# Performance work log

Measured on AMD Instinct MI355X. Metric: run time of the kernel, lower is better.

## Reference

```python
import jax, jax.numpy as jnp
import numpy as np

B, T, C = 2, 2048, 1024
H, D = 16, 64          # n_heads, head_dim
E, K, HD = 8, 2, 1536  # num_experts, active_experts, expert hidden (int(1.5*C))
EPS = 1e-6


def setup_inputs() -> dict:
    key = jax.random.key(0)
    ks = jax.random.split(key, 13)
    s = 0.02
    return {
        "x": jax.random.normal(ks[0], (B, T, C), jnp.float32),
        "rope_cos": jax.random.uniform(ks[1], (T, D), jnp.float32),
        "rope_sin": jax.random.uniform(ks[2], (T, D), jnp.float32),
        "attn_norm_w": jnp.ones((C,), jnp.float32),
        "q_w": jax.random.normal(ks[3], (C, C), jnp.float32) * s,
        "k_w": jax.random.normal(ks[4], (C, C), jnp.float32) * s,
        "v_w": jax.random.normal(ks[5], (C, C), jnp.float32) * s,
        "o_w": jax.random.normal(ks[6], (C, C), jnp.float32) * s,
        "ffn_norm_w": jnp.ones((C,), jnp.float32),
        "router_w": jax.random.normal(ks[7], (E, C), jnp.float32) * s,
        "w1": jax.random.normal(ks[8], (E, HD, C), jnp.float32) * s,
        "w2": jax.random.normal(ks[9], (E, C, HD), jnp.float32) * s,
        "w3": jax.random.normal(ks[10], (E, HD, C), jnp.float32) * s,
    }


def rmsnorm(x, w):
    var = jnp.mean(x * x, axis=-1, keepdims=True)
    return w * x * jax.lax.rsqrt(var + EPS)


def apply_rope(x, cos, sin):
    # x: [B, T, H, D]; cos/sin: [T, D]
    cos = cos[None, :, None, :]
    sin = sin[None, :, None, :]
    d = x.shape[-1] // 2
    x1, x2 = x[..., :d], x[..., d:]
    rotated = jnp.concatenate([-x2, x1], axis=-1)
    return x * cos + rotated * sin


def reference(x, rope_cos, rope_sin, attn_norm_w, q_w, k_w, v_w, o_w,
              ffn_norm_w, router_w, w1, w2, w3):
    b, t, c = x.shape
    h = rmsnorm(x, attn_norm_w)
    q = (h @ q_w.T).reshape(b, t, H, D)
    k = (h @ k_w.T).reshape(b, t, H, D)
    v = (h @ v_w.T).reshape(b, t, H, D)
    q = apply_rope(q, rope_cos[:t], rope_sin[:t]).transpose(0, 2, 1, 3)  # [B,H,T,D]
    k = apply_rope(k, rope_cos[:t], rope_sin[:t]).transpose(0, 2, 1, 3)
    v = v.transpose(0, 2, 1, 3)
    scores = jnp.einsum('bhqd,bhkd->bhqk', q, k) / jnp.sqrt(jnp.asarray(D, q.dtype))
    causal = jnp.tril(jnp.ones((t, t), bool))
    scores = jnp.where(causal, scores, -jnp.inf)
    attn = jax.nn.softmax(scores, axis=-1)
    y = jnp.einsum('bhqk,bhkd->bhqd', attn, v)
    y = y.transpose(0, 2, 1, 3).reshape(b, t, c)
    x = x + y @ o_w.T

    # Sparse MoE (top-K routing, per-expert SwiGLU, weighted combine)
    hn = rmsnorm(x, ffn_norm_w)
    flat = hn.reshape(-1, c)                                # [N, C]
    logits = flat @ router_w.T                              # [N, E]
    wk, idx = jax.lax.top_k(logits, K)                      # [N, K]
    wk = jax.nn.softmax(wk, axis=-1)
    # combined per-expert gate: [N, E] (zero for unrouted experts)
    gate = jnp.sum((idx[..., None] == jnp.arange(E)) * wk[..., None], axis=1)
    out = jnp.zeros_like(flat)
    for e in range(E):
        g = jax.nn.silu(flat @ w1[e].T) * (flat @ w3[e].T)  # [N, HD]
        out = out + gate[:, e:e + 1] * (g @ w2[e].T)
    return x + out.reshape(b, t, c)
```

## Files before the change

### kernel.cpp

```cpp
#include <hip/hip_runtime.h>
#include <hip/hip_bf16.h>
#include <math.h>

#define Bq 2
#define Tq 2048
#define Cq 1024
#define Hq 16
#define Dq 64
#define Eq 8
#define HDq 1536
#define NTOK (Bq*Tq)

typedef unsigned short u16;
typedef _Float16 f16;
typedef __bf16 bf16x8 __attribute__((ext_vector_type(8)));
typedef _Float16 f16x8 __attribute__((ext_vector_type(8)));
typedef float f32x4v __attribute__((ext_vector_type(4)));

#define MB(x) ((size_t)(x) * 262144)

__device__ __forceinline__ float silu_f(float a) {
    return a / (1.0f + __expf(-a));
}
__device__ __forceinline__ u16 f2bf(float f) {
    union { float f; unsigned u; } a; a.f = f;
    unsigned r = a.u + 0x7fffu + ((a.u >> 16) & 1u);
    return (u16)(r >> 16);
}
__device__ __forceinline__ u16 f16bits(f16 h) {
    union { f16 f; u16 u; } a; a.f = h; return a.u;
}

__device__ __forceinline__ void stage16(const void* g, void* l) {
    __builtin_amdgcn_global_load_lds(
        (const __attribute__((address_space(1))) unsigned int*)g,
        (__attribute__((address_space(3))) unsigned int*)l, 16, 0, 0);
}

__global__ __launch_bounds__(256) void rmsnorm_split_k(const float* __restrict__ x,
                                                       const float* __restrict__ w,
                                                       u16* __restrict__ hh,
                                                       u16* __restrict__ hl) {
    int row = blockIdx.x;
    int tid = threadIdx.x;
    const float* xr = x + (size_t)row * Cq;
    float4 v = *(const float4*)(xr + tid * 4);
    float ss = v.x*v.x + v.y*v.y + v.z*v.z + v.w*v.w;
    #pragma unroll
    for (int off = 32; off; off >>= 1) ss += __shfl_xor(ss, off);
    __shared__ float red[4];
    if ((tid & 63) == 0) red[tid >> 6] = ss;
    __syncthreads();
    float tot = red[0] + red[1] + red[2] + red[3];
    float scale = rsqrtf(tot * (1.0f / (float)Cq) + 1e-6f);
    float4 wv = *(const float4*)(w + tid * 4);
    float o[4] = { v.x*wv.x*scale, v.y*wv.y*scale, v.z*wv.z*scale, v.w*wv.w*scale };
    ushort4 oh, ol;
    u16* ph = (u16*)&oh; u16* pl = (u16*)&ol;
    #pragma unroll
    for (int i = 0; i < 4; i++) {
        f16 hi = (f16)o[i]; f16 lo = (f16)(o[i] - (float)hi);
        ph[i] = f16bits(hi); pl[i] = f16bits(lo);
    }
    *(ushort4*)(hh + (size_t)row * Cq + tid * 4) = oh;
    *(ushort4*)(hl + (size_t)row * Cq + tid * 4) = ol;
}

__global__ __launch_bounds__(256) void rmsnorm2_k(const float* __restrict__ x,
                                                  const float* __restrict__ w,
                                                  float* __restrict__ hn,
                                                  u16* __restrict__ hnb) {
    int row = blockIdx.x;
    int tid = threadIdx.x;
    const float* xr = x + (size_t)row * Cq;
    float4 v = *(const float4*)(xr + tid * 4);
    float ss = v.x*v.x + v.y*v.y + v.z*v.z + v.w*v.w;
    #pragma unroll
    for (int off = 32; off; off >>= 1) ss += __shfl_xor(ss, off);
    __shared__ float red[4];
    if ((tid & 63) == 0) red[tid >> 6] = ss;
    __syncthreads();
    float tot = red[0] + red[1] + red[2] + red[3];
    float scale = rsqrtf(tot * (1.0f / (float)Cq) + 1e-6f);
    float4 wv = *(const float4*)(w + tid * 4);
    float4 o = make_float4(v.x*wv.x*scale, v.y*wv.y*scale, v.z*wv.z*scale, v.w*wv.w*scale);
    *(float4*)(hn + (size_t)row * Cq + tid * 4) = o;
    ushort4 ob = make_ushort4(f2bf(o.x), f2bf(o.y), f2bf(o.z), f2bf(o.w));
    *(ushort4*)(hnb + (size_t)row * Cq + tid * 4) = ob;
}

__global__ __launch_bounds__(256, 3) void gemm_fused(const u16* __restrict__ Ahg,
                                                     const u16* __restrict__ Alg,
                                                     const float* __restrict__ Wq,
                                                     const float* __restrict__ Wk,
                                                     const float* __restrict__ Wv,
                                                     u16* __restrict__ qh_o,
                                                     u16* __restrict__ ql_o,
                                                     u16* __restrict__ kh_o,
                                                     u16* __restrict__ kl_o,
                                                     float* __restrict__ vf_o,
                                                     const float* __restrict__ cosb,
                                                     const float* __restrict__ sinb,
                                                     const float* __restrict__ aux,
                                                     float* __restrict__ outf,
                                                     int kind) {
    __shared__ u16 AhS[2][128*32], AlS[2][128*32], BhS[128*32], BlS[128*32];
    int tid = threadIdx.x;
    int wave = tid >> 6, lane = tid & 63;
    int wm = wave >> 1, wn = wave & 1;
    int bx = blockIdx.x, by = blockIdx.y;
    int proj, nx;
    const float* W;
    if (kind == 0) {
        proj = bx >> 3; nx = bx & 7;
        W = (proj == 0) ? Wq : ((proj == 1) ? Wk : Wv);
    } else {
        proj = 3; nx = bx; W = Wq;
    }

    int srow = tid >> 2, sch = (tid & 3) * 8;
    const u16* A0 = Ahg + (size_t)(by*128 + srow) * Cq + sch;
    const u16* A1 = A0 + (size_t)64 * Cq;
    const u16* L0 = Alg + (size_t)(by*128 + srow) * Cq + sch;
    const u16* L1 = L0 + (size_t)64 * Cq;
    const float* W0 = W + (size_t)(nx*128 + srow) * Cq + sch;
    const float* W1 = W0 + (size_t)64 * Cq;
    int lo0 = srow*32 + sch, lo1 = lo0 + 2048;

    f32x4v acc[4][4];
    #pragma unroll
    for (int i = 0; i < 4; i++)
        #pragma unroll
        for (int j = 0; j < 4; j++)
            #pragma unroll
            for (int r = 0; r < 4; r++) acc[i][j][r] = 0.0f;

    float wr0[8], wr1[8];
    stage16(A0, &AhS[0][lo0]);
    stage16(A1, &AhS[0][lo1]);
    stage16(L0, &AlS[0][lo0]);
    stage16(L1, &AlS[0][lo1]);
    *(float4*)&wr0[0] = *(const float4*)(W0);
    *(float4*)&wr0[4] = *(const float4*)(W0 + 4);
    *(float4*)&wr1[0] = *(const float4*)(W1);
    *(float4*)&wr1[4] = *(const float4*)(W1 + 4);

    int fr = lane & 15, fk = (lane >> 4) * 8;
    int cur = 0;
    for (int k0 = 0; k0 < Cq; k0 += 32, cur ^= 1) {
        __syncthreads();
        {
            f16x8 bh0, bl0, bh1, bl1;
            #pragma unroll
            for (int i = 0; i < 8; i++) {
                f16 h0 = (f16)wr0[i]; bh0[i] = h0; bl0[i] = (f16)(wr0[i] - (float)h0);
                f16 h1 = (f16)wr1[i]; bh1[i] = h1; bl1[i] = (f16)(wr1[i] - (float)h1);
            }
            *(f16x8*)(void*)&BhS[lo0] = bh0;
            *(f16x8*)(void*)&BlS[lo0] = bl0;
            *(f16x8*)(void*)&BhS[lo1] = bh1;
            *(f16x8*)(void*)&BlS[lo1] = bl1;
        }
        __syncthreads();
        int kn = k0 + 32;
        if (kn < Cq) {
            stage16(A0 + kn, &AhS[cur^1][lo0]);
            stage16(A1 + kn, &AhS[cur^1][lo1]);
            stage16(L0 + kn, &AlS[cur^1][lo0]);
            stage16(L1 + kn, &AlS[cur^1][lo1]);
            *(float4*)&wr0[0] = *(const float4*)(W0 + kn);
            *(float4*)&wr0[4] = *(const float4*)(W0 + kn + 4);
            *(float4*)&wr1[0] = *(const float4*)(W1 + kn);
            *(float4*)&wr1[4] = *(const float4*)(W1 + kn + 4);
        }
        f16x8 ah[4], al[4];
        #pragma unroll
        for (int mi = 0; mi < 4; mi++) {
            ah[mi] = *(const f16x8*)(const void*)&AhS[cur][(wm*64 + mi*16 + fr)*32 + fk];
            al[mi] = *(const f16x8*)(const void*)&AlS[cur][(wm*64 + mi*16 + fr)*32 + fk];
        }
        #pragma unroll
        for (int ni = 0; ni < 4; ni++) {
            f16x8 bhf = *(const f16x8*)(const void*)&BhS[(wn*64 + ni*16 + fr)*32 + fk];
            f16x8 blf = *(const f16x8*)(const void*)&BlS[(wn*64 + ni*16 + fr)*32 + fk];
            #pragma unroll
            for (int mi = 0; mi < 4; mi++) {
                acc[mi][ni] = __builtin_amdgcn_mfma_f32_16x16x32_f16(ah[mi], bhf, acc[mi][ni], 0, 0, 0);
                acc[mi][ni] = __builtin_amdgcn_mfma_f32_16x16x32_f16(ah[mi], blf, acc[mi][ni], 0, 0, 0);
                acc[mi][ni] = __builtin_amdgcn_mfma_f32_16x16x32_f16(al[mi], bhf, acc[mi][ni], 0, 0, 0);
            }
        }
    }

    int cr = (lane >> 4) * 4, cc = lane & 15;
    if (proj < 2) {
        u16* dh = (proj == 0) ? qh_o : kh_o;
        u16* dl = (proj == 0) ? ql_o : kl_o;
        float scale = (proj == 0) ? 0.125f : 1.0f;
        int hd = (nx * 2 + wn) * 64;
        #pragma unroll
        for (int mi = 0; mi < 4; mi++)
            #pragma unroll
            for (int r = 0; r < 4; r++) {
                int row = by*128 + wm*64 + mi*16 + cr + r;
                int t = row & (Tq - 1);
                #pragma unroll
                for (int ni = 0; ni < 2; ni++) {
                    int d0 = ni*16 + cc;
                    float a = acc[mi][ni][r];
                    float b = acc[mi][ni+2][r];
                    float c0 = cosb[t*Dq + d0],      s0 = sinb[t*Dq + d0];
                    float c1 = cosb[t*Dq + d0 + 32], s1 = sinb[t*Dq + d0 + 32];
                    float oa = (a * c0 - b * s0) * scale;
                    float ob = (b * c1 + a * s1) * scale;
                    size_t off = (size_t)row * Cq + hd + d0;
                    f16 ha = (f16)oa;
                    f16 hb = (f16)ob;
                    dh[off]      = f16bits(ha);
                    dl[off]      = f16bits((f16)(oa - (float)ha));
                    dh[off + 32] = f16bits(hb);
                    dl[off + 32] = f16bits((f16)(ob - (float)hb));
                }
            }
    } else if (proj == 2) {
        #pragma unroll
        for (int mi = 0; mi < 4; mi++)
            #pragma unroll
            for (int r = 0; r < 4; r++) {
                int row = by*128 + wm*64 + mi*16 + cr + r;
                #pragma unroll
                for (int ni = 0; ni < 4; ni++)
                    vf_o[(size_t)row * Cq + nx*128 + wn*64 + ni*16 + cc] = acc[mi][ni][r];
            }
    } else {
        #pragma unroll
        for (int mi = 0; mi < 4; mi++)
            #pragma unroll
            for (int r = 0; r < 4; r++) {
                int row = by*128 + wm*64 + mi*16 + cr + r;
                #pragma unroll
                for (int ni = 0; ni < 4; ni++) {
                    size_t off = (size_t)row * Cq + nx*128 + wn*64 + ni*16 + cc;
                    outf[off] = acc[mi][ni][r] + aux[off];
                }
            }
    }
}

__global__ __launch_bounds__(256) void vtrans_k(const float* __restrict__ v,
                                                u16* __restrict__ vth,
                                                u16* __restrict__ vtl) {
    __shared__ u16 Th[64 * 72];
    __shared__ u16 Tl[64 * 72];
    int tc = blockIdx.x;
    int bh = blockIdx.y;
    int b = bh >> 4, h = bh & 15;
    int tid = threadIdx.x;
    int tr = tid >> 2;
    int dc = (tid & 3) * 16;
    size_t gin = ((size_t)(b * Tq + tc * 64 + tr)) * Cq + h * Dq + dc;
    #pragma unroll
    for (int i = 0; i < 16; i += 4) {
        float4 f = *(const float4*)(v + gin + i);
        float fv[4] = {f.x, f.y, f.z, f.w};
        #pragma unroll
        for (int j = 0; j < 4; j++) {
            f16 hi = (f16)fv[j];
            f16 lo = (f16)(fv[j] - (float)hi);
            Th[(dc + i + j) * 72 + tr] = f16bits(hi);
            Tl[(dc + i + j) * 72 + tr] = f16bits(lo);
        }
    }
    __syncthreads();
    int dr = tid >> 2;
    int cc = (tid & 3) * 16;
    size_t gout = ((size_t)(bh * 64 + dr)) * Tq + tc * 64 + cc;
    *(uint4*)(vth + gout)     = *(uint4*)(Th + dr * 72 + cc);
    *(uint4*)(vth + gout + 8) = *(uint4*)(Th + dr * 72 + cc + 8);
    *(uint4*)(vtl + gout)     = *(uint4*)(Tl + dr * 72 + cc);
    *(uint4*)(vtl + gout + 8) = *(uint4*)(Tl + dr * 72 + cc + 8);
}

#define AST 72
__global__ __launch_bounds__(256, 2) void attn_f16(const u16* __restrict__ qh_g,
                                                   const u16* __restrict__ ql_g,
                                                   const u16* __restrict__ kh_g,
                                                   const u16* __restrict__ kl_g,
                                                   const u16* __restrict__ vth_g,
                                                   const u16* __restrict__ vtl_g,
                                                   u16* __restrict__ yh_g,
                                                   u16* __restrict__ yl_g) {
    __shared__ u16 Qh[64*AST], Ql[64*AST];
    __shared__ u16 Kh[64*AST], Kl[64*AST];
    __shared__ u16 Vh[64*AST], Vl[64*AST];
    __shared__ u16 Ph[64*AST], Pl[64*AST];

    int j  = blockIdx.x;
    int bh = blockIdx.y;
    int b = bh >> 4, h = bh & 15;
    int tid = threadIdx.x;
    int wv = tid >> 6, lane = tid & 63;
    int fr = lane & 15, fg = lane >> 4;
    int sr = tid >> 2, sc = (tid & 3) * 16;
    int aoff = (wv * 16 + fr) * AST + fg * 8;

    uint4 rkh0, rkh1, rkl0, rkl1, rvh0, rvh1, rvl0, rvl1;
    auto ldkv = [&](int kt) {
        size_t kg = ((size_t)(b * Tq + kt * 64 + sr)) * Cq + h * Dq + sc;
        size_t vg = ((size_t)(bh * 64 + sr)) * Tq + kt * 64 + sc;
        rkh0 = *(const uint4*)(kh_g + kg);  rkh1 = *(const uint4*)(kh_g + kg + 8);
        rkl0 = *(const uint4*)(kl_g + kg);  rkl1 = *(const uint4*)(kl_g + kg + 8);
        rvh0 = *(const uint4*)(vth_g + vg); rvh1 = *(const uint4*)(vth_g + vg + 8);
        rvl0 = *(const uint4*)(vtl_g + vg); rvl1 = *(const uint4*)(vtl_g + vg + 8);
    };

    #pragma unroll
    for (int pass = 0; pass < 2; pass++) {
        int qt = pass == 0 ? (31 - j) : j;

        __syncthreads();
        {
            size_t g = ((size_t)(b * Tq + qt * 64 + sr)) * Cq + h * Dq + sc;
            *(uint4*)(Qh + sr*AST + sc)     = *(const uint4*)(qh_g + g);
            *(uint4*)(Qh + sr*AST + sc + 8) = *(const uint4*)(qh_g + g + 8);
            *(uint4*)(Ql + sr*AST + sc)     = *(const uint4*)(ql_g + g);
            *(uint4*)(Ql + sr*AST + sc + 8) = *(const uint4*)(ql_g + g + 8);
        }
        ldkv(0);

        f32x4v acc_o[4];
        float m_i[4], l_i[4];
        #pragma unroll
        for (int i = 0; i < 4; i++) {
            m_i[i] = -1e30f; l_i[i] = 0.0f;
            #pragma unroll
            for (int r = 0; r < 4; r++) acc_o[i][r] = 0.0f;
        }

        for (int kt = 0; kt <= qt; kt++) {
            __syncthreads();
            *(uint4*)(Kh + sr*AST + sc)     = rkh0;
            *(uint4*)(Kh + sr*AST + sc + 8) = rkh1;
            *(uint4*)(Kl + sr*AST + sc)     = rkl0;
            *(uint4*)(Kl + sr*AST + sc + 8) = rkl1;
            *(uint4*)(Vh + sr*AST + sc)     = rvh0;
            *(uint4*)(Vh + sr*AST + sc + 8) = rvh1;
            *(uint4*)(Vl + sr*AST + sc)     = rvl0;
            *(uint4*)(Vl + sr*AST + sc + 8) = rvl1;
            __syncthreads();
            if (kt < qt) ldkv(kt + 1);

            f16x8 aqh0 = *(const f16x8*)(const void*)(Qh + aoff);
            f16x8 aqh1 = *(const f16x8*)(const void*)(Qh + aoff + 32);
            f16x8 aql0 = *(const f16x8*)(const void*)(Ql + aoff);
            f16x8 aql1 = *(const f16x8*)(const void*)(Ql + aoff + 32);

            f32x4v s[4];
            #pragma unroll
            for (int ni = 0; ni < 4; ni++) {
                int boff = (ni * 16 + fr) * AST + fg * 8;
                f16x8 kh0 = *(const f16x8*)(const void*)(Kh + boff);
                f16x8 kh1 = *(const f16x8*)(const void*)(Kh + boff + 32);
                f16x8 kl0 = *(const f16x8*)(const void*)(Kl + boff);
                f16x8 kl1 = *(const f16x8*)(const void*)(Kl + boff + 32);
                f32x4v t;
                #pragma unroll
                for (int r = 0; r < 4; r++) t[r] = 0.0f;
                t = __builtin_amdgcn_mfma_f32_16x16x32_f16(aqh0, kh0, t, 0, 0, 0);
                t = __builtin_amdgcn_mfma_f32_16x16x32_f16(aqh1, kh1, t, 0, 0, 0);
                t = __builtin_amdgcn_mfma_f32_16x16x32_f16(aqh0, kl0, t, 0, 0, 0);
                t = __builtin_amdgcn_mfma_f32_16x16x32_f16(aqh1, kl1, t, 0, 0, 0);
                t = __builtin_amdgcn_mfma_f32_16x16x32_f16(aql0, kh0, t, 0, 0, 0);
                t = __builtin_amdgcn_mfma_f32_16x16x32_f16(aql1, kh1, t, 0, 0, 0);
                s[ni] = t;
            }

            if (kt == qt) {
                #pragma unroll
                for (int ni = 0; ni < 4; ni++) {
                    int col = ni * 16 + fr;
                    #pragma unroll
                    for (int r = 0; r < 4; r++) {
                        int row = wv * 16 + fg * 4 + r;
                        if (col > row) s[ni][r] = -1e30f;
                    }
                }
            }

            float p[4][4];
            #pragma unroll
            for (int r = 0; r < 4; r++) {
                float mx = fmaxf(fmaxf(s[0][r], s[1][r]), fmaxf(s[2][r], s[3][r]));
                #pragma unroll
                for (int off = 1; off < 16; off <<= 1)
                    mx = fmaxf(mx, __shfl_xor(mx, off, 16));
                float mn = fmaxf(m_i[r], mx);
                float rs = 0.0f;
                #pragma unroll
                for (int ni = 0; ni < 4; ni++) {
                    p[ni][r] = __expf(s[ni][r] - mn);
                    rs += p[ni][r];
                }
                #pragma unroll
                for (int off = 1; off < 16; off <<= 1)
                    rs += __shfl_xor(rs, off, 16);
                float alpha = __expf(m_i[r] - mn);
                l_i[r] = l_i[r] * alpha + rs;
                m_i[r] = mn;
                #pragma unroll
                for (int ni = 0; ni < 4; ni++) acc_o[ni][r] *= alpha;
            }

            #pragma unroll
            for (int ni = 0; ni < 4; ni++) {
                #pragma unroll
                for (int r = 0; r < 4; r++) {
                    int off = (wv * 16 + fg * 4 + r) * AST + ni * 16 + fr;
                    f16 ph = (f16)p[ni][r];
                    f16 pl = (f16)(p[ni][r] - (float)ph);
                    Ph[off] = f16bits(ph);
                    Pl[off] = f16bits(pl);
                }
            }

            f16x8 aph0 = *(const f16x8*)(const void*)(Ph + aoff);
            f16x8 aph1 = *(const f16x8*)(const void*)(Ph + aoff + 32);
            f16x8 apl0 = *(const f16x8*)(const void*)(Pl + aoff);
            f16x8 apl1 = *(const f16x8*)(const void*)(Pl + aoff + 32);
            #pragma unroll
            for (int ni = 0; ni < 4; ni++) {
                int boff = (ni * 16 + fr) * AST + fg * 8;
                f16x8 vh0 = *(const f16x8*)(const void*)(Vh + boff);
                f16x8 vh1 = *(const f16x8*)(const void*)(Vh + boff + 32);
                f16x8 vl0 = *(const f16x8*)(const void*)(Vl + boff);
                f16x8 vl1 = *(const f16x8*)(const void*)(Vl + boff + 32);
                f32x4v t = acc_o[ni];
                t = __builtin_amdgcn_mfma_f32_16x16x32_f16(aph0, vh0, t, 0, 0, 0);
                t = __builtin_amdgcn_mfma_f32_16x16x32_f16(aph1, vh1, t, 0, 0, 0);
                t = __builtin_amdgcn_mfma_f32_16x16x32_f16(aph0, vl0, t, 0, 0, 0);
                t = __builtin_amdgcn_mfma_f32_16x16x32_f16(aph1, vl1, t, 0, 0, 0);
                t = __builtin_amdgcn_mfma_f32_16x16x32_f16(apl0, vh0, t, 0, 0, 0);
                t = __builtin_amdgcn_mfma_f32_16x16x32_f16(apl1, vh1, t, 0, 0, 0);
                acc_o[ni] = t;
            }
        }

        #pragma unroll
        for (int r = 0; r < 4; r++) {
            float inv = 1.0f / l_i[r];
            int row = qt * 64 + wv * 16 + fg * 4 + r;
            size_t base = ((size_t)(b * Tq + row)) * Cq + h * Dq + fr;
            #pragma unroll
            for (int ni = 0; ni < 4; ni++) {
                float yv = acc_o[ni][r] * inv;
                f16 hi = (f16)yv;
                f16 lo = (f16)(yv - (float)hi);
                yh_g[base + ni * 16] = f16bits(hi);
                yl_g[base + ni * 16] = f16bits(lo);
            }
        }
    }
}

__global__ void zero_k(int* cnt) {
    if (threadIdx.x < Eq) cnt[threadIdx.x] = 0;
}

__global__ __launch_bounds__(64) void router_k(const float* __restrict__ hn,
                                               const float* __restrict__ rw,
                                               int* __restrict__ cnt,
                                               int* __restrict__ idxl,
                                               float* __restrict__ gvl) {
    int tkn = blockIdx.x;
    int lane = threadIdx.x;
    float acc[Eq] = {};
    for (int it = 0; it < Cq / 64; it++) {
        float hv = hn[(size_t)tkn * Cq + it * 64 + lane];
        #pragma unroll
        for (int e = 0; e < Eq; e++)
            acc[e] = fmaf(hv, rw[e * Cq + it * 64 + lane], acc[e]);
    }
    #pragma unroll
    for (int e = 0; e < Eq; e++) {
        #pragma unroll
        for (int off = 32; off; off >>= 1) acc[e] += __shfl_xor(acc[e], off);
    }
    int i0 = 0;
    #pragma unroll
    for (int e = 1; e < Eq; e++) if (acc[e] > acc[i0]) i0 = e;
    int i1 = (i0 == 0) ? 1 : 0;
    #pragma unroll
    for (int e = 0; e < Eq; e++)
        if (e != i0 && acc[e] > acc[i1]) i1 = e;
    float p1 = __expf(acc[i1] - acc[i0]);
    float g0 = 1.0f / (1.0f + p1);
    float g1 = p1 / (1.0f + p1);
    if (lane == 0) {
        int p0 = atomicAdd(&cnt[i0], 1);
        idxl[i0 * NTOK + p0] = tkn;
        gvl[i0 * NTOK + p0] = g0;
        int p1i = atomicAdd(&cnt[i1], 1);
        idxl[i1 * NTOK + p1i] = tkn;
        gvl[i1 * NTOK + p1i] = g1;
    }
}

__global__ void setup_k(const int* __restrict__ cnt, int* __restrict__ seg,
                        int* __restrict__ texp, int* __restrict__ ttot) {
    if (threadIdx.x == 0) {
        int base = 0;
        for (int e = 0; e < Eq; e++) {
            seg[e] = base * 128;
            int t = (cnt[e] + 127) >> 7;
            for (int i = 0; i < t; i++) texp[base + i] = e;
            base += t;
        }
        *ttot = base;
    }
}

__global__ __launch_bounds__(256, 2) void moe_w13(const u16* __restrict__ hnb,
                                                  const float* __restrict__ w1,
                                                  const float* __restrict__ w3,
                                                  u16* __restrict__ gbuf,
                                                  const int* __restrict__ cnt,
                                                  const int* __restrict__ seg,
                                                  const int* __restrict__ texp,
                                                  const int* __restrict__ ttot,
                                                  const int* __restrict__ idxl) {
    int by = blockIdx.y;
    if (by >= *ttot) return;
    int e = texp[by];
    const float* w1e = w1 + (size_t)e * HDq * Cq;
    const float* w3e = w3 + (size_t)e * HDq * Cq;
    int cnte = cnt[e], sege = seg[e];
    const int* idxe = idxl + e * NTOK;

    __shared__ u16 As[2][128*32], B1S[128*32], B3S[128*32];
    int tid = threadIdx.x;
    int wave = tid >> 6, lane = tid & 63;
    int wm = wave >> 1, wn = wave & 1;
    int bx = blockIdx.x;
    int srow = tid >> 2, sch = (tid & 3) * 8;

    int r0 = by*128 + srow, r1 = r0 + 64;
    int li0 = r0 - sege, li1 = r1 - sege;
    int tok0 = idxe[li0 < cnte ? li0 : 0];
    int tok1 = idxe[li1 < cnte ? li1 : 0];
    const u16* A0 = hnb + (size_t)tok0 * Cq + sch;
    const u16* A1 = hnb + (size_t)tok1 * Cq + sch;
    const float* W10 = w1e + (size_t)(bx*128 + srow) * Cq + sch;
    const float* W11 = W10 + (size_t)64 * Cq;
    const float* W30 = w3e + (size_t)(bx*128 + srow) * Cq + sch;
    const float* W31 = W30 + (size_t)64 * Cq;
    int lo0 = srow*32 + sch, lo1 = lo0 + 2048;

    f32x4v acc1[4][4], acc3[4][4];
    #pragma unroll
    for (int i = 0; i < 4; i++)
        #pragma unroll
        for (int j = 0; j < 4; j++)
            #pragma unroll
            for (int r = 0; r < 4; r++) { acc1[i][j][r] = 0.0f; acc3[i][j][r] = 0.0f; }

    float x1a[8], x1b[8], x3a[8], x3b[8];
    stage16(A0, &As[0][lo0]);
    stage16(A1, &As[0][lo1]);
    *(float4*)&x1a[0] = *(const float4*)(W10);
    *(float4*)&x1a[4] = *(const float4*)(W10 + 4);
    *(float4*)&x1b[0] = *(const float4*)(W11);
    *(float4*)&x1b[4] = *(const float4*)(W11 + 4);
    *(float4*)&x3a[0] = *(const float4*)(W30);
    *(float4*)&x3a[4] = *(const float4*)(W30 + 4);
    *(float4*)&x3b[0] = *(const float4*)(W31);
    *(float4*)&x3b[4] = *(const float4*)(W31 + 4);

    int fr = lane & 15, fk = (lane >> 4) * 8;
    int cur = 0;
    for (int k0 = 0; k0 < Cq; k0 += 32, cur ^= 1) {
        __syncthreads();
        {
            u16 t0[8], t1[8], t2[8], t3[8];
            #pragma unroll
            for (int i = 0; i < 8; i++) {
                t0[i] = f2bf(x1a[i]); t1[i] = f2bf(x1b[i]);
                t2[i] = f2bf(x3a[i]); t3[i] = f2bf(x3b[i]);
            }
            *(uint4*)&B1S[lo0] = *(uint4*)t0;
            *(uint4*)&B1S[lo1] = *(uint4*)t1;
            *(uint4*)&B3S[lo0] = *(uint4*)t2;
            *(uint4*)&B3S[lo1] = *(uint4*)t3;
        }
        __syncthreads();
        int kn = k0 + 32;
        if (kn < Cq) {
            stage16(A0 + kn, &As[cur^1][lo0]);
            stage16(A1 + kn, &As[cur^1][lo1]);
            *(float4*)&x1a[0] = *(const float4*)(W10 + kn);
            *(float4*)&x1a[4] = *(const float4*)(W10 + kn + 4);
            *(float4*)&x1b[0] = *(const float4*)(W11 + kn);
            *(float4*)&x1b[4] = *(const float4*)(W11 + kn + 4);
            *(float4*)&x3a[0] = *(const float4*)(W30 + kn);
            *(float4*)&x3a[4] = *(const float4*)(W30 + kn + 4);
            *(float4*)&x3b[0] = *(const float4*)(W31 + kn);
            *(float4*)&x3b[4] = *(const float4*)(W31 + kn + 4);
        }
        bf16x8 af[4];
        #pragma unroll
        for (int mi = 0; mi < 4; mi++)
            af[mi] = *(const bf16x8*)&As[cur][(wm*64 + mi*16 + fr) * 32 + fk];
        #pragma unroll
        for (int ni = 0; ni < 4; ni++) {
            bf16x8 b1f = *(const bf16x8*)&B1S[(wn*64 + ni*16 + fr) * 32 + fk];
            bf16x8 b3f = *(const bf16x8*)&B3S[(wn*64 + ni*16 + fr) * 32 + fk];
            #pragma unroll
            for (int mi = 0; mi < 4; mi++) {
                acc1[mi][ni] = __builtin_amdgcn_mfma_f32_16x16x32_bf16(af[mi], b1f, acc1[mi][ni], 0, 0, 0);
                acc3[mi][ni] = __builtin_amdgcn_mfma_f32_16x16x32_bf16(af[mi], b3f, acc3[mi][ni], 0, 0, 0);
            }
        }
    }

    int cr = (lane >> 4) * 4, cc = lane & 15;
    #pragma unroll
    for (int mi = 0; mi < 4; mi++)
        #pragma unroll
        for (int ni = 0; ni < 4; ni++)
            #pragma unroll
            for (int r = 0; r < 4; r++) {
                int row = by*128 + wm*64 + mi*16 + cr + r;
                int col = bx*128 + wn*64 + ni*16 + cc;
                gbuf[(size_t)row * HDq + col] = f2bf(silu_f(acc1[mi][ni][r]) * acc3[mi][ni][r]);
            }
}

__global__ __launch_bounds__(256, 3) void moe_w2(const u16* __restrict__ gbuf,
                                                 const float* __restrict__ w2,
                                                 float* __restrict__ out,
                                                 const int* __restrict__ cnt,
                                                 const int* __restrict__ seg,
                                                 const int* __restrict__ texp,
                                                 const int* __restrict__ ttot,
                                                 const int* __restrict__ idxl,
                                                 const float* __restrict__ gvl) {
    int by = blockIdx.y;
    if (by >= *ttot) return;
    int e = texp[by];
    const float* w2e = w2 + (size_t)e * Cq * HDq;
    int cnte = cnt[e], sege = seg[e];
    const int* idxe = idxl + e * NTOK;
    const float* gve = gvl + e * NTOK;

    __shared__ u16 As[2][128*32], Bs[128*32];
    int tid = threadIdx.x;
    int wave = tid >> 6, lane = tid & 63;
    int wm = wave >> 1, wn = wave & 1;
    int bx = blockIdx.x;
    int srow = tid >> 2, sch = (tid & 3) * 8;

    const u16* A0 = gbuf + (size_t)(by*128 + srow) * HDq + sch;
    const u16* A1 = A0 + (size_t)64 * HDq;
    const float* W0 = w2e + (size_t)(bx*128 + srow) * HDq + sch;
    const float* W1 = W0 + (size_t)64 * HDq;
    int lo0 = srow*32 + sch, lo1 = lo0 + 2048;

    f32x4v acc[4][4];
    #pragma unroll
    for (int i = 0; i < 4; i++)
        #pragma unroll
        for (int j = 0; j < 4; j++)
            #pragma unroll
            for (int r = 0; r < 4; r++) acc[i][j][r] = 0.0f;

    float xa[8], xb[8];
    stage16(A0, &As[0][lo0]);
    stage16(A1, &As[0][lo1]);
    *(float4*)&xa[0] = *(const float4*)(W0);
    *(float4*)&xa[4] = *(const float4*)(W0 + 4);
    *(float4*)&xb[0] = *(const float4*)(W1);
    *(float4*)&xb[4] = *(const float4*)(W1 + 4);

    int fr = lane & 15, fk = (lane >> 4) * 8;
    int cur = 0;
    for (int k0 = 0; k0 < HDq; k0 += 32, cur ^= 1) {
        __syncthreads();
        {
            u16 ta[8], tb[8];
            #pragma unroll
            for (int i = 0; i < 8; i++) { ta[i] = f2bf(xa[i]); tb[i] = f2bf(xb[i]); }
            *(uint4*)&Bs[lo0] = *(uint4*)ta;
            *(uint4*)&Bs[lo1] = *(uint4*)tb;
        }
        __syncthreads();
        int kn = k0 + 32;
        if (kn < HDq) {
            stage16(A0 + kn, &As[cur^1][lo0]);
            stage16(A1 + kn, &As[cur^1][lo1]);
            *(float4*)&xa[0] = *(const float4*)(W0 + kn);
            *(float4*)&xa[4] = *(const float4*)(W0 + kn + 4);
            *(float4*)&xb[0] = *(const float4*)(W1 + kn);
            *(float4*)&xb[4] = *(const float4*)(W1 + kn + 4);
        }
        bf16x8 af[4];
        #pragma unroll
        for (int mi = 0; mi < 4; mi++)
            af[mi] = *(const bf16x8*)&As[cur][(wm*64 + mi*16 + fr) * 32 + fk];
        #pragma unroll
        for (int ni = 0; ni < 4; ni++) {
            bf16x8 bf_ = *(const bf16x8*)&Bs[(wn*64 + ni*16 + fr) * 32 + fk];
            #pragma unroll
            for (int mi = 0; mi < 4; mi++)
                acc[mi][ni] = __builtin_amdgcn_mfma_f32_16x16x32_bf16(af[mi], bf_, acc[mi][ni], 0, 0, 0);
        }
    }

    int cr = (lane >> 4) * 4, cc = lane & 15;
    #pragma unroll
    for (int mi = 0; mi < 4; mi++)
        #pragma unroll
        for (int r = 0; r < 4; r++) {
            int row = by*128 + wm*64 + mi*16 + cr + r;
            int local = row - sege;
            if (local < cnte) {
                int token = idxe[local];
                float g = gve[local];
                #pragma unroll
                for (int ni = 0; ni < 4; ni++) {
                    int col = bx*128 + wn*64 + ni*16 + cc;
                    atomicAdd(&out[(size_t)token * Cq + col], g * acc[mi][ni][r]);
                }
            }
        }
}

extern "C" void kernel_launch(void* const* d_in, const int* in_sizes, int n_in,
                              void* d_out, int out_size, void* d_ws, size_t ws_size,
                              hipStream_t stream) {
    (void)in_sizes; (void)n_in; (void)out_size; (void)ws_size;

    const float* x     = (const float*)d_in[0];
    const float* ropec = (const float*)d_in[1];
    const float* ropes = (const float*)d_in[2];
    const float* anw   = (const float*)d_in[3];
    const float* q_w   = (const float*)d_in[4];
    const float* k_w   = (const float*)d_in[5];
    const float* v_w   = (const float*)d_in[6];
    const float* o_w   = (const float*)d_in[7];
    const float* fnw   = (const float*)d_in[8];
    const float* rtw   = (const float*)d_in[9];
    const float* w1    = (const float*)d_in[10];
    const float* w2    = (const float*)d_in[11];
    const float* w3    = (const float*)d_in[12];
    float* out = (float*)d_out;

    float* ws = (float*)d_ws;
    u16* hh = (u16*)(ws + MB(0));
    u16* hl = (u16*)(ws + MB(8));
    float* vf = ws + MB(16);
    u16* qh = (u16*)(ws + MB(32));
    u16* ql = (u16*)(ws + MB(40));
    u16* kh = (u16*)(ws + MB(48));
    u16* kl = (u16*)(ws + MB(56));
    u16* vth = (u16*)(ws + MB(0));
    u16* vtl = (u16*)(ws + MB(8));
    u16* yh  = (u16*)(ws + MB(16));
    u16* yl  = (u16*)(ws + MB(24));
    u16* gbuf = (u16*)(ws + MB(0));
    float* hn = ws + MB(32);
    u16* hnb  = (u16*)(ws + MB(48));
    int* cntp = (int*)(ws + MB(56));
    int* segp = cntp + 8;
    int* texp = cntp + 16;
    int* ttot = cntp + 96;
    int* idxl = cntp + 256;
    float* gvl = (float*)(cntp + 256 + Eq*NTOK);

    const int M = NTOK;

    hipLaunchKernelGGL(rmsnorm_split_k, dim3(M), dim3(256), 0, stream, x, anw, hh, hl);

    hipLaunchKernelGGL(gemm_fused, dim3(24, M/128), dim3(256), 0, stream,
                       hh, hl, q_w, k_w, v_w, qh, ql, kh, kl, vf,
                       ropec, ropes, (const float*)nullptr, (float*)nullptr, 0);

    hipLaunchKernelGGL(vtrans_k, dim3(32, 32), dim3(256), 0, stream, vf, vth, vtl);

    hipLaunchKernelGGL(attn_f16, dim3(16, Bq*Hq), dim3(256), 0, stream,
                       qh, ql, kh, kl, vth, vtl, yh, yl);

    hipLaunchKernelGGL(gemm_fused, dim3(8, M/128), dim3(256), 0, stream,
                       yh, yl, o_w, (const float*)nullptr, (const float*)nullptr,
                       (u16*)nullptr, (u16*)nullptr, (u16*)nullptr, (u16*)nullptr,
                       (float*)nullptr, ropec, ropes, x, out, 1);

    hipLaunchKernelGGL(rmsnorm2_k, dim3(M), dim3(256), 0, stream, out, fnw, hn, hnb);

    hipLaunchKernelGGL(zero_k, dim3(1), dim3(64), 0, stream, cntp);
    hipLaunchKernelGGL(router_k, dim3(M), dim3(64), 0, stream, hn, rtw, cntp, idxl, gvl);
    hipLaunchKernelGGL(setup_k, dim3(1), dim3(64), 0, stream, cntp, segp, texp, ttot);

    hipLaunchKernelGGL(moe_w13, dim3(HDq/128, 72), dim3(256), 0, stream,
                       hnb, w1, w3, gbuf, cntp, segp, texp, ttot, idxl);
    hipLaunchKernelGGL(moe_w2, dim3(Cq/128, 72), dim3(256), 0, stream,
                       gbuf, w2, out, cntp, segp, texp, ttot, idxl, gvl);
}
```

Measured before the change: 753.1 us.

## Pre-convert MoE expert weights to bf16 and use bf16-weight MoE GEMMs

Adds a kernel that converts w1, w3 and w2 from fp32 to bf16 into workspace, run on every call. New MoE GEMM kernels then stage the bf16 weights directly with double-buffered shared memory for both A and B, instead of converting fp32 weights inside the GEMM. This aims to halve weight bandwidth in the GEMMs and remove in-loop conversion, at the cost of an extra pass that reads about 150MB of fp32 and writes bf16. The new path runs only when the workspace is large enough.

```diff
diff --git a/kernel.cpp b/kernel.cpp
--- a/kernel.cpp
+++ b/kernel.cpp
@@ -87,6 +87,24 @@
     *(float4*)(hn + (size_t)row * Cq + tid * 4) = o;
     ushort4 ob = make_ushort4(f2bf(o.x), f2bf(o.y), f2bf(o.z), f2bf(o.w));
     *(ushort4*)(hnb + (size_t)row * Cq + tid * 4) = ob;
+}
+
+__global__ __launch_bounds__(256) void wconv_k(const float* __restrict__ w1,
+                                               const float* __restrict__ w3,
+                                               const float* __restrict__ w2,
+                                               u16* __restrict__ w1b,
+                                               u16* __restrict__ w3b,
+                                               u16* __restrict__ w2b) {
+    int a = blockIdx.y;
+    const float* src = (a == 0) ? w1 : ((a == 1) ? w3 : w2);
+    u16* dst = (a == 0) ? w1b : ((a == 1) ? w3b : w2b);
+    size_t i = ((size_t)blockIdx.x * 256 + threadIdx.x) * 8;
+    float4 f0 = *(const float4*)(src + i);
+    float4 f1 = *(const float4*)(src + i + 4);
+    ushort4 o0 = make_ushort4(f2bf(f0.x), f2bf(f0.y), f2bf(f0.z), f2bf(f0.w));
+    ushort4 o1 = make_ushort4(f2bf(f1.x), f2bf(f1.y), f2bf(f1.z), f2bf(f1.w));
+    *(ushort4*)(dst + i)     = o0;
+    *(ushort4*)(dst + i + 4) = o1;
 }
 
 __global__ __launch_bounds__(256, 3) void gemm_fused(const u16* __restrict__ Ahg,
@@ -519,6 +537,175 @@
     }
 }
 
+__global__ __launch_bounds__(256, 2) void moe_w13b(const u16* __restrict__ hnb,
+                                                   const u16* __restrict__ w1b,
+                                                   const u16* __restrict__ w3b,
+                                                   u16* __restrict__ gbuf,
+                                                   const int* __restrict__ cnt,
+                                                   const int* __restrict__ seg,
+                                                   const int* __restrict__ texp,
+                                                   const int* __restrict__ ttot,
+                                                   const int* __restrict__ idxl) {
+    int by = blockIdx.y;
+    if (by >= *ttot) return;
+    int e = texp[by];
+    const u16* w1e = w1b + (size_t)e * HDq * Cq;
+    const u16* w3e = w3b + (size_t)e * HDq * Cq;
+    int cnte = cnt[e], sege = seg[e];
+    const int* idxe = idxl + e * NTOK;
+
+    __shared__ u16 As[2][128*32], B1S[2][128*32], B3S[2][128*32];
+    int tid = threadIdx.x;
+    int wave = tid >> 6, lane = tid & 63;
+    int wm = wave >> 1, wn = wave & 1;
+    int bx = blockIdx.x;
+    int srow = tid >> 2, sch = (tid & 3) * 8;
+
+    int r0 = by*128 + srow, r1 = r0 + 64;
+    int li0 = r0 - sege, li1 = r1 - sege;
+    int tok0 = idxe[li0 < cnte ? li0 : 0];
+    int tok1 = idxe[li1 < cnte ? li1 : 0];
+    const u16* A0 = hnb + (size_t)tok0 * Cq + sch;
+    const u16* A1 = hnb + (size_t)tok1 * Cq + sch;
+    const u16* W10 = w1e + (size_t)(bx*128 + srow) * Cq + sch;
+    const u16* W11 = W10 + (size_t)64 * Cq;
+    const u16* W30 = w3e + (size_t)(bx*128 + srow) * Cq + sch;
+    const u16* W31 = W30 + (size_t)64 * Cq;
+    int lo0 = srow*32 + sch, lo1 = lo0 + 2048;
+
+    f32x4v acc1[4][4], acc3[4][4];
+    #pragma unroll
+    for (int i = 0; i < 4; i++)
+        #pragma unroll
+        for (int j = 0; j < 4; j++)
+            #pragma unroll
+            for (int r = 0; r < 4; r++) { acc1[i][j][r] = 0.0f; acc3[i][j][r] = 0.0f; }
+
+    stage16(A0,  &As[0][lo0]);  stage16(A1,  &As[0][lo1]);
+    stage16(W10, &B1S[0][lo0]); stage16(W11, &B1S[0][lo1]);
+    stage16(W30, &B3S[0][lo0]); stage16(W31, &B3S[0][lo1]);
+
+    int fr = lane & 15, fk = (lane >> 4) * 8;
+    int cur = 0;
+    for (int k0 = 0; k0 < Cq; k0 += 32, cur ^= 1) {
+        __syncthreads();
+        int kn = k0 + 32;
+        if (kn < Cq) {
+            stage16(A0 + kn,  &As[cur^1][lo0]);  stage16(A1 + kn,  &As[cur^1][lo1]);
+            stage16(W10 + kn, &B1S[cur^1][lo0]); stage16(W11 + kn, &B1S[cur^1][lo1]);
+            stage16(W30 + kn, &B3S[cur^1][lo0]); stage16(W31 + kn, &B3S[cur^1][lo1]);
+        }
+        bf16x8 af[4];
+        #pragma unroll
+        for (int mi = 0; mi < 4; mi++)
+            af[mi] = *(const bf16x8*)&As[cur][(wm*64 + mi*16 + fr) * 32 + fk];
+        #pragma unroll
+        for (int ni = 0; ni < 4; ni++) {
+            bf16x8 b1f = *(const bf16x8*)&B1S[cur][(wn*64 + ni*16 + fr) * 32 + fk];
+            bf16x8 b3f = *(const bf16x8*)&B3S[cur][(wn*64 + ni*16 + fr) * 32 + fk];
+            #pragma unroll
+            for (int mi = 0; mi < 4; mi++) {
+                acc1[mi][ni] = __builtin_amdgcn_mfma_f32_16x16x32_bf16(af[mi], b1f, acc1[mi][ni], 0, 0, 0);
+                acc3[mi][ni] = __builtin_amdgcn_mfma_f32_16x16x32_bf16(af[mi], b3f, acc3[mi][ni], 0, 0, 0);
+            }
+        }
+    }
+
+    int cr = (lane >> 4) * 4, cc = lane & 15;
+    #pragma unroll
+    for (int mi = 0; mi < 4; mi++)
+        #pragma unroll
+        for (int ni = 0; ni < 4; ni++)
+            #pragma unroll
+            for (int r = 0; r < 4; r++) {
+                int row = by*128 + wm*64 + mi*16 + cr + r;
+                int col = bx*128 + wn*64 + ni*16 + cc;
+                gbuf[(size_t)row * HDq + col] = f2bf(silu_f(acc1[mi][ni][r]) * acc3[mi][ni][r]);
+            }
+}
+
+__global__ __launch_bounds__(256, 3) void moe_w2b_k(const u16* __restrict__ gbuf,
+                                                    const u16* __restrict__ w2b,
+                                                    float* __restrict__ out,
+                                                    const int* __restrict__ cnt,
+                                                    const int* __restrict__ seg,
+                                                    const int* __restrict__ texp,
+                                                    const int* __restrict__ ttot,
+                                                    const int* __restrict__ idxl,
+                                                    const float* __restrict__ gvl) {
+    int by = blockIdx.y;
+    if (by >= *ttot) return;
+    int e = texp[by];
+    const u16* w2e = w2b + (size_t)e * Cq * HDq;
+    int cnte = cnt[e], sege = seg[e];
+    const int* idxe = idxl + e * NTOK;
+    const float* gve = gvl + e * NTOK;
+
+    __shared__ u16 As[2][128*32], Bs[2][128*32];
+    int tid = threadIdx.x;
+    int wave = tid >> 6, lane = tid & 63;
+    int wm = wave >> 1, wn = wave & 1;
+    int bx = blockIdx.x;
+    int srow = tid >> 2, sch = (tid & 3) * 8;
+
+    const u16* A0 = gbuf + (size_t)(by*128 + srow) * HDq + sch;
+    const u16* A1 = A0 + (size_t)64 * HDq;
+    const u16* W0 = w2e + (size_t)(bx*128 + srow) * HDq + sch;
+    const u16* W1 = W0 + (size_t)64 * HDq;
+    int lo0 = srow*32 + sch, lo1 = lo0 + 2048;
+
+    f32x4v acc[4][4];
+    #pragma unroll
+    for (int i = 0; i < 4; i++)
+        #pragma unroll
+        for (int j = 0; j < 4; j++)
+            #pragma unroll
+            for (int r = 0; r < 4; r++) acc[i][j][r] = 0.0f;
+
+    stage16(A0, &As[0][lo0]); stage16(A1, &As[0][lo1]);
+    stage16(W0, &Bs[0][lo0]); stage16(W1, &Bs[0][lo1]);
+
+    int fr = lane & 15, fk = (lane >> 4) * 8;
+    int cur = 0;
+    for (int k0 = 0; k0 < HDq; k0 += 32, cur ^= 1) {
+        __syncthreads();
+        int kn = k0 + 32;
+        if (kn < HDq) {
+            stage16(A0 + kn, &As[cur^1][lo0]); stage16(A1 + kn, &As[cur^1][lo1]);
+            stage16(W0 + kn, &Bs[cur^1][lo0]); stage16(W1 + kn, &Bs[cur^1][lo1]);
+        }
+        bf16x8 af[4];
+        #pragma unroll
+        for (int mi = 0; mi < 4; mi++)
+            af[mi] = *(const bf16x8*)&As[cur][(wm*64 + mi*16 + fr) * 32 + fk];
+        #pragma unroll
+        for (int ni = 0; ni < 4; ni++) {
+            bf16x8 bf_ = *(const bf16x8*)&Bs[cur][(wn*64 + ni*16 + fr) * 32 + fk];
+            #pragma unroll
+            for (int mi = 0; mi < 4; mi++)
+                acc[mi][ni] = __builtin_amdgcn_mfma_f32_16x16x32_bf16(af[mi], bf_, acc[mi][ni], 0, 0, 0);
+        }
+    }
+
+    int cr = (lane >> 4) * 4, cc = lane & 15;
+    #pragma unroll
+    for (int mi = 0; mi < 4; mi++)
+        #pragma unroll
+        for (int r = 0; r < 4; r++) {
+            int row = by*128 + wm*64 + mi*16 + cr + r;
+            int local = row - sege;
+            if (local < cnte) {
+                int token = idxe[local];
+                float g = gve[local];
+                #pragma unroll
+                for (int ni = 0; ni < 4; ni++) {
+                    int col = bx*128 + wn*64 + ni*16 + cc;
+                    atomicAdd(&out[(size_t)token * Cq + col], g * acc[mi][ni][r]);
+                }
+            }
+        }
+}
+
 __global__ __launch_bounds__(256, 2) void moe_w13(const u16* __restrict__ hnb,
                                                   const float* __restrict__ w1,
                                                   const float* __restrict__ w3,
@@ -736,7 +923,7 @@
 extern "C" void kernel_launch(void* const* d_in, const int* in_sizes, int n_in,
                               void* d_out, int out_size, void* d_ws, size_t ws_size,
                               hipStream_t stream) {
-    (void)in_sizes; (void)n_in; (void)out_size; (void)ws_size;
+    (void)in_sizes; (void)n_in; (void)out_size;
 
     const float* x     = (const float*)d_in[0];
     const float* ropec = (const float*)d_in[1];
@@ -774,8 +961,16 @@
     int* ttot = cntp + 96;
     int* idxl = cntp + 256;
     float* gvl = (float*)(cntp + 256 + Eq*NTOK);
+    u16* w1b = (u16*)(ws + MB(64));
+    u16* w3b = (u16*)(ws + MB(88));
+    u16* w2b = (u16*)(ws + MB(112));
 
     const int M = NTOK;
+    const bool pre = ws_size >= ((size_t)136 << 20);
+
+    if (pre)
+        hipLaunchKernelGGL(wconv_k, dim3(6144, 3), dim3(256), 0, stream,
+                           w1, w3, w2, w1b, w3b, w2b);
 
     hipLaunchKernelGGL(rmsnorm_split_k, dim3(M), dim3(256), 0, stream, x, anw, hh, hl);
 
@@ -799,8 +994,15 @@
     hipLaunchKernelGGL(router_k, dim3(M), dim3(64), 0, stream, hn, rtw, cntp, idxl, gvl);
     hipLaunchKernelGGL(setup_k, dim3(1), dim3(64), 0, stream, cntp, segp, texp, ttot);
 
-    hipLaunchKernelGGL(moe_w13, dim3(HDq/128, 72), dim3(256), 0, stream,
-                       hnb, w1, w3, gbuf, cntp, segp, texp, ttot, idxl);
-    hipLaunchKernelGGL(moe_w2, dim3(Cq/128, 72), dim3(256), 0, stream,
-                       gbuf, w2, out, cntp, segp, texp, ttot, idxl, gvl);
-}
+    if (pre) {
+        hipLaunchKernelGGL(moe_w13b, dim3(HDq/128, 72), dim3(256), 0, stream,
+                           hnb, w1b, w3b, gbuf, cntp, segp, texp, ttot, idxl);
+        hipLaunchKernelGGL(moe_w2b_k, dim3(Cq/128, 72), dim3(256), 0, stream,
+                           gbuf, w2b, out, cntp, segp, texp, ttot, idxl, gvl);
+    } else {
+        hipLaunchKernelGGL(moe_w13, dim3(HDq/128, 72), dim3(256), 0, stream,
+                           hnb, w1, w3, gbuf, cntp, segp, texp, ttot, idxl);
+        hipLaunchKernelGGL(moe_w2, dim3(Cq/128, 72), dim3(256), 0, stream,
+                           gbuf, w2, out, cntp, segp, texp, ttot, idxl, gvl);
+    }
+}
```

After: 721.1 us. -4.2%, faster.
